# Performance work log

Hardware: AMD Instinct MI355X
Metric: run time of the kernel (lower is better)

The kernel has to match this reference:

```python
import jax, jax.numpy as jnp
import numpy as np

N_NODES = 50000


def _gin_conv(x, src, dst, w1, b1, w2, b2):
    # sum-aggregate neighbor features: agg[i] = sum_{(j->i) in E} x[j]
    agg = jax.ops.segment_sum(x[src], dst, num_segments=N_NODES)
    h = x + agg  # eps = 0 (PyG GINConv default, not trainable)
    h = jnp.maximum(h @ w1 + b1, 0.0) @ w2 + b2
    return h


def setup_inputs() -> dict:
    key = jax.random.key(0)
    ks = jax.random.split(key, 10)
    d_in, d_h, d_out = 128, 256, 2
    E = 600000
    x = jax.random.normal(ks[0], (N_NODES, d_in), dtype=jnp.float32)
    edge_index = jax.random.randint(ks[1], (2, E), 0, N_NODES, dtype=jnp.int64)
    s = lambda k, sh: jax.random.normal(k, sh, dtype=jnp.float32) * (1.0 / np.sqrt(sh[0]))
    return {
        "x": x,
        "edge_index": edge_index,
        "w1": s(ks[2], (d_in, d_h)), "b1": jnp.zeros((d_h,), jnp.float32),
        "w2": s(ks[3], (d_h, d_h)), "b2": jnp.zeros((d_h,), jnp.float32),
        "w3": s(ks[4], (d_h, d_h)), "b3": jnp.zeros((d_h,), jnp.float32),
        "w4": s(ks[5], (d_h, d_out)), "b4": jnp.zeros((d_out,), jnp.float32),
    }


def reference(x, edge_index, w1, b1, w2, b2, w3, b3, w4, b4):
    src, dst = edge_index[0], edge_index[1]
    h = _gin_conv(x, src, dst, w1, b1, w2, b2)
    h = jnp.maximum(h, 0.0)  # F.relu between the two GINConv layers
    h = _gin_conv(h, src, dst, w3, b3, w4, b4)
    return jax.nn.log_softmax(h, axis=1)
```

## Files before the change

kernel.cpp:

```cpp
#include <hip/hip_runtime.h>
#include <hip/hip_bf16.h>


typedef __attribute__((ext_vector_type(8))) short bf16x8;
typedef __attribute__((ext_vector_type(4))) float f32x4;

static __device__ __forceinline__ unsigned short f2bf(float f) {
    unsigned int u = __float_as_uint(f);
    unsigned int r = (u + 0x7fffu + ((u >> 16) & 1u)) >> 16;
    return (unsigned short)r;
}
static __device__ __forceinline__ float bf2f(unsigned short s) {
    return __uint_as_float(((unsigned int)s) << 16);
}
static __device__ __forceinline__ float bflo(unsigned int u) {
    return __uint_as_float(u << 16);
}
static __device__ __forceinline__ float bfhi(unsigned int u) {
    return __uint_as_float(u & 0xffff0000u);
}

#define S1 136
#define S2 264

static __device__ __forceinline__ void acc8(float* a, uint2 v, float ss) {
    a[0] = fmaf(ss, (float)( v.x        & 0xff), a[0]);
    a[1] = fmaf(ss, (float)((v.x >> 8 ) & 0xff), a[1]);
    a[2] = fmaf(ss, (float)((v.x >> 16) & 0xff), a[2]);
    a[3] = fmaf(ss, (float)( v.x >> 24        ), a[3]);
    a[4] = fmaf(ss, (float)( v.y        & 0xff), a[4]);
    a[5] = fmaf(ss, (float)((v.y >> 8 ) & 0xff), a[5]);
    a[6] = fmaf(ss, (float)((v.y >> 16) & 0xff), a[6]);
    a[7] = fmaf(ss, (float)( v.y >> 24        ), a[7]);
}

__global__ __launch_bounds__(256) void prep_kernel(
    const float* __restrict__ x,
    unsigned char* __restrict__ x_q, float* __restrict__ xscale,
    const float* __restrict__ w1, const float* __restrict__ w2, const float* __restrict__ w3,
    short* __restrict__ w1t, short* __restrict__ w2t, short* __restrict__ w3t,
    const int* __restrict__ dst, int* __restrict__ deg,
    int M, int E, int cB)
{
    const int b = blockIdx.x;
    const int t = threadIdx.x;
    if (b < cB) {
        const int i = b * 256 + t;
        const int n4 = M * 32;
        if (i >= n4) return;
        const float4 v = *(const float4*)(x + (size_t)i * 4);
        float mx = fmaxf(fmaxf(fabsf(v.x), fabsf(v.y)), fmaxf(fabsf(v.z), fabsf(v.w)));
        #pragma unroll
        for (int o2 = 1; o2 < 32; o2 <<= 1)
            mx = fmaxf(mx, __shfl_xor(mx, o2));
        const float inv = (mx > 0.f) ? 127.f / mx : 0.f;
        uchar4 o;
        o.x = (unsigned char)(int)(v.x * inv + 128.5f);
        o.y = (unsigned char)(int)(v.y * inv + 128.5f);
        o.z = (unsigned char)(int)(v.z * inv + 128.5f);
        o.w = (unsigned char)(int)(v.w * inv + 128.5f);
        const int row = i >> 5;
        *(uchar4*)(x_q + (size_t)row * 128 + (i & 31) * 4) = o;
        if ((t & 31) == 0) xscale[row] = (mx > 0.f) ? mx * (1.f / 127.f) : 0.f;
        return;
    }
    if (b < cB + 192) {
        const int tb = b - cB;
        const int z = tb >> 6;
        const int rem = tb & 63;
        const int kb = rem & 7;
        const int nb = rem >> 3;
        const float* in; short* outb; int K, ostride;
        if (z == 0)      { in = w1; outb = w1t; K = 128; ostride = S1; }
        else if (z == 1) { in = w2; outb = w2t; K = 256; ostride = S2; }
        else             { in = w3; outb = w3t; K = 256; ostride = S2; }
        const int N = 256;
        const int k0 = kb * 32;
        if (k0 >= K) return;
        const int n0 = nb * 32;
        __shared__ float tile[32][33];
        const int tx = t & 31;
        const int ty = t >> 5;
        #pragma unroll
        for (int i = 0; i < 4; ++i)
            tile[ty + 8 * i][tx] = in[(size_t)(k0 + ty + 8 * i) * N + n0 + tx];
        __syncthreads();
        #pragma unroll
        for (int i = 0; i < 4; ++i)
            outb[(size_t)(n0 + ty + 8 * i) * ostride + k0 + tx] = (short)f2bf(tile[tx][ty + 8 * i]);
        return;
    }
    const int e = (b - cB - 192) * 256 + t;
    if (e < E) atomicAdd(&deg[dst[e]], 1);
}

__global__ __launch_bounds__(256) void block_sum_kernel(
    const int* __restrict__ deg, int* __restrict__ bsum, int M)
{
    const int b = blockIdx.x, t = threadIdx.x;
    const int idx = b * 1024 + t * 4;
    int s = 0;
    if (idx + 3 < M) {
        const int4 v = *(const int4*)(deg + idx);
        s = v.x + v.y + v.z + v.w;
    } else {
        #pragma unroll
        for (int i = 0; i < 4; ++i) if (idx + i < M) s += deg[idx + i];
    }
    #pragma unroll
    for (int off = 32; off > 0; off >>= 1) s += __shfl_down(s, off);
    __shared__ int ws[4];
    if ((t & 63) == 0) ws[t >> 6] = s;
    __syncthreads();
    if (t == 0) bsum[b] = ws[0] + ws[1] + ws[2] + ws[3];
}

__global__ __launch_bounds__(256) void scan_blocks2_kernel(
    const int* __restrict__ deg, const int* __restrict__ bsum,
    int* __restrict__ rowptr, int* __restrict__ cur, int M, int E, int nB)
{
    const int b = blockIdx.x, t = threadIdx.x;
    __shared__ int sboff;
    if (t < 64) {
        const int v = (t < nB) ? bsum[t] : 0;
        int inc = v;
        #pragma unroll
        for (int off = 1; off < 64; off <<= 1) {
            const int u = __shfl_up(inc, off);
            if (t >= off) inc += u;
        }
        const int prev = __shfl(inc, (b == 0) ? 0 : (b - 1));
        if (t == 0) sboff = (b == 0) ? 0 : prev;
    }
    const int idx = b * 1024 + t * 4;
    int4 d = make_int4(0, 0, 0, 0);
    if (idx + 3 < M) {
        d = *(const int4*)(deg + idx);
    } else {
        if (idx + 0 < M) d.x = deg[idx + 0];
        if (idx + 1 < M) d.y = deg[idx + 1];
        if (idx + 2 < M) d.z = deg[idx + 2];
        if (idx + 3 < M) d.w = deg[idx + 3];
    }
    const int tot = d.x + d.y + d.z + d.w;
    const int lane = t & 63, wid = t >> 6;
    int inc = tot;
    #pragma unroll
    for (int off = 1; off < 64; off <<= 1) {
        const int u = __shfl_up(inc, off);
        if (lane >= off) inc += u;
    }
    __shared__ int wsum[4];
    if (lane == 63) wsum[wid] = inc;
    __syncthreads();
    int woff = 0;
    #pragma unroll
    for (int w = 0; w < 4; ++w) if (w < wid) woff += wsum[w];
    int p = sboff + woff + (inc - tot);
    if (idx + 0 < M) { rowptr[idx + 0] = p; cur[idx + 0] = p; } p += d.x;
    if (idx + 1 < M) { rowptr[idx + 1] = p; cur[idx + 1] = p; } p += d.y;
    if (idx + 2 < M) { rowptr[idx + 2] = p; cur[idx + 2] = p; } p += d.z;
    if (idx + 3 < M) { rowptr[idx + 3] = p; cur[idx + 3] = p; }
    if (b == 0 && t == 0) rowptr[M] = E;
}

__global__ __launch_bounds__(256) void fill_kernel(
    const int* __restrict__ src, const int* __restrict__ dst,
    int* __restrict__ cur, int* __restrict__ srcs, int E)
{
    const int e = blockIdx.x * 256 + threadIdx.x;
    if (e >= E) return;
    const int p = atomicAdd(&cur[dst[e]], 1);
    srcs[p] = src[e];
}

__global__ __launch_bounds__(256) void gather_add_d128q(
    const unsigned char* __restrict__ x_q,
    const float* __restrict__ xscale,
    const int* __restrict__ rowptr, const int* __restrict__ srcs,
    short* __restrict__ outb, int M)
{
    const int row = blockIdx.x * 4 + (threadIdx.x >> 6);
    if (row >= M) return;
    const int lane = threadIdx.x & 63;
    const int qt = lane >> 4;
    const int o = (lane & 15) * 8;
    float a[8];
    #pragma unroll
    for (int k = 0; k < 8; ++k) a[k] = 0.f;
    float ssum = 0.f;
    if (qt == 0) {
        const uint2 u = *(const uint2*)(x_q + (size_t)row * 128 + o);
        const float sc = xscale[row];
        acc8(a, u, sc);
        ssum += sc;
    }
    const int jb = rowptr[row], je = rowptr[row + 1];
    for (int j = jb; j < je; j += 16) {
        int ss[4];
        #pragma unroll
        for (int t = 0; t < 4; ++t)
            ss[t] = srcs[min(j + 4 * t + qt, je - 1)];
        uint2 v[4]; float sc[4];
        #pragma unroll
        for (int t = 0; t < 4; ++t) {
            v[t] = *(const uint2*)(x_q + (size_t)ss[t] * 128 + o);
            const float scv = xscale[ss[t]];
            sc[t] = (j + 4 * t + qt < je) ? scv : 0.f;
        }
        #pragma unroll
        for (int t = 0; t < 4; ++t) { acc8(a, v[t], sc[t]); ssum += sc[t]; }
    }
    #pragma unroll
    for (int k = 0; k < 8; ++k) a[k] = fmaf(-128.f, ssum, a[k]);
    #pragma unroll
    for (int k = 0; k < 8; ++k) {
        a[k] += __shfl_down(a[k], 16);
        a[k] += __shfl_down(a[k], 32);
    }
    if (qt == 0) {
        uint4 up;
        up.x = (unsigned int)f2bf(a[0]) | ((unsigned int)f2bf(a[1]) << 16);
        up.y = (unsigned int)f2bf(a[2]) | ((unsigned int)f2bf(a[3]) << 16);
        up.z = (unsigned int)f2bf(a[4]) | ((unsigned int)f2bf(a[5]) << 16);
        up.w = (unsigned int)f2bf(a[6]) | ((unsigned int)f2bf(a[7]) << 16);
        *(uint4*)(outb + (size_t)row * S1 + o) = up;
    }
}

__global__ __launch_bounds__(256) void gather_add_d256q(
    const unsigned char* __restrict__ h1q,
    const float* __restrict__ hscale,
    const int* __restrict__ rowptr, const int* __restrict__ srcs,
    short* __restrict__ outb, int M)
{
    const int row = blockIdx.x * 4 + (threadIdx.x >> 6);
    if (row >= M) return;
    const int lane = threadIdx.x & 63;
    const int half = lane >> 5;
    const int o = (lane & 31) * 8;
    float a[8];
    #pragma unroll
    for (int k = 0; k < 8; ++k) a[k] = 0.f;
    if (half == 0) {
        const uint2 u = *(const uint2*)(h1q + (size_t)row * 256 + o);
        acc8(a, u, hscale[row]);
    }
    const int jb = rowptr[row], je = rowptr[row + 1];
    for (int j = jb; j < je; j += 16) {
        int ss[8];
        #pragma unroll
        for (int t = 0; t < 8; ++t)
            ss[t] = srcs[min(j + 2 * t + half, je - 1)];
        uint2 v[8]; float sc[8];
        #pragma unroll
        for (int t = 0; t < 8; ++t) {
            v[t] = *(const uint2*)(h1q + (size_t)ss[t] * 256 + o);
            const float scv = hscale[ss[t]];
            sc[t] = (j + 2 * t + half < je) ? scv : 0.f;
        }
        #pragma unroll
        for (int t = 0; t < 8; ++t) acc8(a, v[t], sc[t]);
    }
    #pragma unroll
    for (int k = 0; k < 8; ++k) a[k] += __shfl_down(a[k], 32);
    if (half == 0) {
        uint4 up;
        up.x = (unsigned int)f2bf(a[0]) | ((unsigned int)f2bf(a[1]) << 16);
        up.y = (unsigned int)f2bf(a[2]) | ((unsigned int)f2bf(a[3]) << 16);
        up.z = (unsigned int)f2bf(a[4]) | ((unsigned int)f2bf(a[5]) << 16);
        up.w = (unsigned int)f2bf(a[6]) | ((unsigned int)f2bf(a[7]) << 16);
        *(uint4*)(outb + (size_t)row * S2 + o) = up;
    }
}

__global__ __launch_bounds__(256) void layer1_fused(
    const short* __restrict__ h1in,
    const short* __restrict__ w1t,
    const float* __restrict__ b1,
    const short* __restrict__ w2t,
    const float* __restrict__ b2,
    unsigned char* __restrict__ h1q,
    float* __restrict__ hscale,
    int M)
{
    __shared__ short sT[64 * S2];
    __shared__ float sMax[64][4];
    __shared__ float sInv[64];
    const int tid  = threadIdx.x;
    const int lane = tid & 63;
    const int wid  = tid >> 6;
    const int r16  = lane & 15;
    const int q    = lane >> 4;
    const int tm   = blockIdx.x * 64;
    const int wn   = wid * 64;

    {
        const short* Aslice = h1in + (size_t)tm * S1;
        #pragma unroll
        for (int c = 0; c < 5; ++c) {
            const int idx = tid + c * 256;
            if (idx < 64 * S1 / 8) {
                const uint4 v = *(const uint4*)(Aslice + idx * 8);
                *(uint4*)(&sT[idx * 8]) = v;
            }
        }
    }
    __syncthreads();

    f32x4 acc[4][4];
    #pragma unroll
    for (int i = 0; i < 4; ++i)
        #pragma unroll
        for (int j = 0; j < 4; ++j)
            acc[i][j] = (f32x4)0.f;

    #pragma unroll
    for (int k0 = 0; k0 < 128; k0 += 32) {
        bf16x8 af[4], bfr[4];
        #pragma unroll
        for (int i = 0; i < 4; ++i)
            af[i] = *(const bf16x8*)(&sT[(i * 16 + r16) * S1 + k0 + q * 8]);
        #pragma unroll
        for (int j = 0; j < 4; ++j)
            bfr[j] = *(const bf16x8*)(w1t + (size_t)(wn + j * 16 + r16) * S1 + k0 + q * 8);
        #pragma unroll
        for (int i = 0; i < 4; ++i)
            #pragma unroll
            for (int j = 0; j < 4; ++j)
                acc[i][j] = __builtin_amdgcn_mfma_f32_16x16x32_bf16(af[i], bfr[j], acc[i][j], 0, 0, 0);
    }
    __syncthreads();

    #pragma unroll
    for (int j = 0; j < 4; ++j) {
        const int col = wn + j * 16 + r16;
        const float bj = b1[col];
        #pragma unroll
        for (int i = 0; i < 4; ++i)
            #pragma unroll
            for (int r = 0; r < 4; ++r) {
                float v = fmaxf(acc[i][j][r] + bj, 0.f);
                sT[(i * 16 + q * 4 + r) * S2 + col] = (short)f2bf(v);
            }
    }
    __syncthreads();

    #pragma unroll
    for (int i = 0; i < 4; ++i)
        #pragma unroll
        for (int j = 0; j < 4; ++j)
            acc[i][j] = (f32x4)0.f;

    #pragma unroll
    for (int k0 = 0; k0 < 256; k0 += 32) {
        bf16x8 af[4], bfr[4];
        #pragma unroll
        for (int i = 0; i < 4; ++i)
            af[i] = *(const bf16x8*)(&sT[(i * 16 + r16) * S2 + k0 + q * 8]);
        #pragma unroll
        for (int j = 0; j < 4; ++j)
            bfr[j] = *(const bf16x8*)(w2t + (size_t)(wn + j * 16 + r16) * S2 + k0 + q * 8);
        #pragma unroll
        for (int i = 0; i < 4; ++i)
            #pragma unroll
            for (int j = 0; j < 4; ++j)
                acc[i][j] = __builtin_amdgcn_mfma_f32_16x16x32_bf16(af[i], bfr[j], acc[i][j], 0, 0, 0);
    }
    __syncthreads();

    {
        float bj4[4];
        #pragma unroll
        for (int j = 0; j < 4; ++j) bj4[j] = b2[wn + j * 16 + r16];
        #pragma unroll
        for (int i = 0; i < 4; ++i) {
            #pragma unroll
            for (int r = 0; r < 4; ++r) {
                float m = 0.f;
                #pragma unroll
                for (int j = 0; j < 4; ++j) {
                    float v = fmaxf(acc[i][j][r] + bj4[j], 0.f);
                    sT[(i * 16 + q * 4 + r) * S2 + wn + j * 16 + r16] = (short)f2bf(v);
                    m = fmaxf(m, v);
                }
                #pragma unroll
                for (int off = 1; off < 16; off <<= 1)
                    m = fmaxf(m, __shfl_xor(m, off));
                if (r16 == 0) sMax[i * 16 + q * 4 + r][wid] = m;
            }
        }
    }
    __syncthreads();

    if (tid < 64) {
        const float m = fmaxf(fmaxf(sMax[tid][0], sMax[tid][1]),
                              fmaxf(sMax[tid][2], sMax[tid][3]));
        sInv[tid] = (m > 0.f) ? 255.f / m : 0.f;
        const int rg = tm + tid;
        if (rg < M) hscale[rg] = m * (1.f / 255.f);
    }
    __syncthreads();

    #pragma unroll
    for (int c = 0; c < 8; ++c) {
        const int idx = tid + c * 256;
        const int row = idx >> 5;
        const int ch  = idx & 31;
        const int rg  = tm + row;
        if (rg < M) {
            const uint4 v = *(const uint4*)(&sT[row * S2 + ch * 8]);
            const float inv = sInv[row];
            unsigned int q0 = min(255u, (unsigned int)(bflo(v.x) * inv + 0.5f));
            unsigned int q1 = min(255u, (unsigned int)(bfhi(v.x) * inv + 0.5f));
            unsigned int q2 = min(255u, (unsigned int)(bflo(v.y) * inv + 0.5f));
            unsigned int q3 = min(255u, (unsigned int)(bfhi(v.y) * inv + 0.5f));
            unsigned int q4 = min(255u, (unsigned int)(bflo(v.z) * inv + 0.5f));
            unsigned int q5 = min(255u, (unsigned int)(bfhi(v.z) * inv + 0.5f));
            unsigned int q6 = min(255u, (unsigned int)(bflo(v.w) * inv + 0.5f));
            unsigned int q7 = min(255u, (unsigned int)(bfhi(v.w) * inv + 0.5f));
            uint2 o8;
            o8.x = q0 | (q1 << 8) | (q2 << 16) | (q3 << 24);
            o8.y = q4 | (q5 << 8) | (q6 << 16) | (q7 << 24);
            *(uint2*)(h1q + (size_t)rg * 256 + ch * 8) = o8;
        }
    }
}

__global__ __launch_bounds__(256) void layer2_fused(
    const short* __restrict__ h2in,
    const short* __restrict__ w3t,
    const float* __restrict__ b3,
    const float* __restrict__ w4,
    const float* __restrict__ b4,
    float* __restrict__ out,
    int M)
{
    __shared__ short sT[64 * S2];
    const int tid  = threadIdx.x;
    const int lane = tid & 63;
    const int wid  = tid >> 6;
    const int r16  = lane & 15;
    const int q    = lane >> 4;
    const int tm   = blockIdx.x * 64;
    const int wn   = wid * 64;

    {
        const short* Aslice = h2in + (size_t)tm * S2;
        #pragma unroll
        for (int c = 0; c < 9; ++c) {
            const int idx = tid + c * 256;
            if (idx < 64 * S2 / 8) {
                const uint4 v = *(const uint4*)(Aslice + idx * 8);
                *(uint4*)(&sT[idx * 8]) = v;
            }
        }
    }
    __syncthreads();

    f32x4 acc[4][4];
    #pragma unroll
    for (int i = 0; i < 4; ++i)
        #pragma unroll
        for (int j = 0; j < 4; ++j)
            acc[i][j] = (f32x4)0.f;

    #pragma unroll
    for (int k0 = 0; k0 < 256; k0 += 32) {
        bf16x8 af[4], bfr[4];
        #pragma unroll
        for (int i = 0; i < 4; ++i)
            af[i] = *(const bf16x8*)(&sT[(i * 16 + r16) * S2 + k0 + q * 8]);
        #pragma unroll
        for (int j = 0; j < 4; ++j)
            bfr[j] = *(const bf16x8*)(w3t + (size_t)(wn + j * 16 + r16) * S2 + k0 + q * 8);
        #pragma unroll
        for (int i = 0; i < 4; ++i)
            #pragma unroll
            for (int j = 0; j < 4; ++j)
                acc[i][j] = __builtin_amdgcn_mfma_f32_16x16x32_bf16(af[i], bfr[j], acc[i][j], 0, 0, 0);
    }
    __syncthreads();

    #pragma unroll
    for (int j = 0; j < 4; ++j) {
        const int col = wn + j * 16 + r16;
        const float bj = b3[col];
        #pragma unroll
        for (int i = 0; i < 4; ++i)
            #pragma unroll
            for (int r = 0; r < 4; ++r) {
                float v = fmaxf(acc[i][j][r] + bj, 0.f);
                sT[(i * 16 + q * 4 + r) * S2 + col] = (short)f2bf(v);
            }
    }
    __syncthreads();

    const int row = tid >> 2;
    const int qd  = tid & 3;
    const short* tp = &sT[row * S2 + qd * 64];
    const float* w4p = w4 + qd * 128;
    float s0 = 0.f, s1 = 0.f;
    #pragma unroll 8
    for (int k = 0; k < 64; ++k) {
        const float a = bf2f((unsigned short)tp[k]);
        const float2 w = *(const float2*)(w4p + 2 * k);
        s0 = fmaf(a, w.x, s0);
        s1 = fmaf(a, w.y, s1);
    }
    s0 += __shfl_down(s0, 2, 4);  s1 += __shfl_down(s1, 2, 4);
    s0 += __shfl_down(s0, 1, 4);  s1 += __shfl_down(s1, 1, 4);
    if (qd == 0) {
        const int rg = tm + row;
        if (rg < M) {
            s0 += b4[0];
            s1 += b4[1];
            const float m = fmaxf(s0, s1);
            const float l = logf(__expf(s0 - m) + __expf(s1 - m));
            float2 o;
            o.x = s0 - m - l;
            o.y = s1 - m - l;
            *(float2*)(out + (size_t)rg * 2) = o;
        }
    }
}

extern "C" void kernel_launch(void* const* d_in, const int* in_sizes, int n_in,
                              void* d_out, int out_size, void* d_ws, size_t ws_size,
                              hipStream_t stream)
{
    const float* x  = (const float*)d_in[0];
    const int*   ei = (const int*)d_in[1];
    const float* w1 = (const float*)d_in[2];
    const float* b1 = (const float*)d_in[3];
    const float* w2 = (const float*)d_in[4];
    const float* b2 = (const float*)d_in[5];
    const float* w3 = (const float*)d_in[6];
    const float* b3 = (const float*)d_in[7];
    const float* w4 = (const float*)d_in[8];
    const float* b4 = (const float*)d_in[9];

    const int DIN = 128, DH = 256;
    const int M = in_sizes[0] / DIN;
    const int E = in_sizes[1] / 2;
    const int* src = ei;
    const int* dst = ei + E;
    const int nB = (M + 1023) / 1024;

    int* deg    = (int*)d_ws;
    int* bsum   = deg + M;
    int* cur    = bsum + 64;
    int* rowptr = cur + M;
    int* srcs   = rowptr + (M + 1);
    size_t off = ((size_t)(3 * M + 1 + 64 + E) * sizeof(int) + 255) & ~(size_t)255;
    unsigned char* x_q = (unsigned char*)((char*)d_ws + off);  off += (size_t)M * 128;
    off = (off + 255) & ~(size_t)255;
    float* xscale = (float*)((char*)d_ws + off);  off += (size_t)M * 4;
    off = (off + 255) & ~(size_t)255;
    short* h1in = (short*)((char*)d_ws + off);  off += (size_t)M * S1 * 2;
    off = (off + 255) & ~(size_t)255;
    unsigned char* h1q = (unsigned char*)((char*)d_ws + off);  off += (size_t)M * 256;
    off = (off + 255) & ~(size_t)255;
    float* hscale = (float*)((char*)d_ws + off);  off += (size_t)M * 4;
    off = (off + 255) & ~(size_t)255;
    short* h2in = (short*)((char*)d_ws + off);  off += (size_t)M * S2 * 2;
    off = (off + 255) & ~(size_t)255;
    short* w1t  = (short*)((char*)d_ws + off);  off += (size_t)DH * S1 * 2;
    off = (off + 255) & ~(size_t)255;
    short* w2t  = (short*)((char*)d_ws + off);  off += (size_t)DH * S2 * 2;
    off = (off + 255) & ~(size_t)255;
    short* w3t  = (short*)((char*)d_ws + off);  off += (size_t)DH * S2 * 2;

    hipMemsetAsync(deg, 0, (size_t)M * sizeof(int), stream);
    const int cB = (M * 32 + 255) / 256;
    const int dB = (E + 255) / 256;
    prep_kernel<<<cB + 192 + dB, 256, 0, stream>>>(
        x, x_q, xscale, w1, w2, w3, w1t, w2t, w3t, dst, deg, M, E, cB);

    block_sum_kernel<<<nB, 256, 0, stream>>>(deg, bsum, M);
    scan_blocks2_kernel<<<nB, 256, 0, stream>>>(deg, bsum, rowptr, cur, M, E, nB);
    fill_kernel<<<dB, 256, 0, stream>>>(src, dst, cur, srcs, E);

    const int nblk = (M + 63) / 64;

    gather_add_d128q<<<(M + 3) / 4, 256, 0, stream>>>(x_q, xscale, rowptr, srcs, h1in, M);
    layer1_fused<<<nblk, 256, 0, stream>>>(h1in, w1t, b1, w2t, b2, h1q, hscale, M);

    gather_add_d256q<<<(M + 3) / 4, 256, 0, stream>>>(h1q, hscale, rowptr, srcs, h2in, M);
    layer2_fused<<<nblk, 256, 0, stream>>>(h2in, w3t, b3, w4, b4, (float*)d_out, M);
}
```

Measured before the change: 271.8 us.

## Fuse neighbor gather-aggregation into layer MLP kernels via shared memory

Moves the sparse gather-sum for each layer into the corresponding fused MLP kernel, so each block aggregates its 64 rows directly into shared memory instead of writing bf16 intermediates to global memory and reading them back. This removes two kernel launches and the global round-trip of the h1in/h2in buffers. In exchange, each wave now processes 16 rows serially with less parallelism per row and fewer concurrent memory requests in flight, and the gather's latency is no longer overlapped by a separate high-occupancy kernel.

```diff
diff --git a/kernel.cpp b/kernel.cpp
--- a/kernel.cpp
+++ b/kernel.cpp
@@ -174,108 +174,10 @@
     srcs[p] = src[e];
 }
 
-__global__ __launch_bounds__(256) void gather_add_d128q(
+__global__ __launch_bounds__(256) void layer1_fused(
     const unsigned char* __restrict__ x_q,
     const float* __restrict__ xscale,
     const int* __restrict__ rowptr, const int* __restrict__ srcs,
-    short* __restrict__ outb, int M)
-{
-    const int row = blockIdx.x * 4 + (threadIdx.x >> 6);
-    if (row >= M) return;
-    const int lane = threadIdx.x & 63;
-    const int qt = lane >> 4;
-    const int o = (lane & 15) * 8;
-    float a[8];
-    #pragma unroll
-    for (int k = 0; k < 8; ++k) a[k] = 0.f;
-    float ssum = 0.f;
-    if (qt == 0) {
-        const uint2 u = *(const uint2*)(x_q + (size_t)row * 128 + o);
-        const float sc = xscale[row];
-        acc8(a, u, sc);
-        ssum += sc;
-    }
-    const int jb = rowptr[row], je = rowptr[row + 1];
-    for (int j = jb; j < je; j += 16) {
-        int ss[4];
-        #pragma unroll
-        for (int t = 0; t < 4; ++t)
-            ss[t] = srcs[min(j + 4 * t + qt, je - 1)];
-        uint2 v[4]; float sc[4];
-        #pragma unroll
-        for (int t = 0; t < 4; ++t) {
-            v[t] = *(const uint2*)(x_q + (size_t)ss[t] * 128 + o);
-            const float scv = xscale[ss[t]];
-            sc[t] = (j + 4 * t + qt < je) ? scv : 0.f;
-        }
-        #pragma unroll
-        for (int t = 0; t < 4; ++t) { acc8(a, v[t], sc[t]); ssum += sc[t]; }
-    }
-    #pragma unroll
-    for (int k = 0; k < 8; ++k) a[k] = fmaf(-128.f, ssum, a[k]);
-    #pragma unroll
-    for (int k = 0; k < 8; ++k) {
-        a[k] += __shfl_down(a[k], 16);
-        a[k] += __shfl_down(a[k], 32);
-    }
-    if (qt == 0) {
-        uint4 up;
-        up.x = (unsigned int)f2bf(a[0]) | ((unsigned int)f2bf(a[1]) << 16);
-        up.y = (unsigned int)f2bf(a[2]) | ((unsigned int)f2bf(a[3]) << 16);
-        up.z = (unsigned int)f2bf(a[4]) | ((unsigned int)f2bf(a[5]) << 16);
-        up.w = (unsigned int)f2bf(a[6]) | ((unsigned int)f2bf(a[7]) << 16);
-        *(uint4*)(outb + (size_t)row * S1 + o) = up;
-    }
-}
-
-__global__ __launch_bounds__(256) void gather_add_d256q(
-    const unsigned char* __restrict__ h1q,
-    const float* __restrict__ hscale,
-    const int* __restrict__ rowptr, const int* __restrict__ srcs,
-    short* __restrict__ outb, int M)
-{
-    const int row = blockIdx.x * 4 + (threadIdx.x >> 6);
-    if (row >= M) return;
-    const int lane = threadIdx.x & 63;
-    const int half = lane >> 5;
-    const int o = (lane & 31) * 8;
-    float a[8];
-    #pragma unroll
-    for (int k = 0; k < 8; ++k) a[k] = 0.f;
-    if (half == 0) {
-        const uint2 u = *(const uint2*)(h1q + (size_t)row * 256 + o);
-        acc8(a, u, hscale[row]);
-    }
-    const int jb = rowptr[row], je = rowptr[row + 1];
-    for (int j = jb; j < je; j += 16) {
-        int ss[8];
-        #pragma unroll
-        for (int t = 0; t < 8; ++t)
-            ss[t] = srcs[min(j + 2 * t + half, je - 1)];
-        uint2 v[8]; float sc[8];
-        #pragma unroll
-        for (int t = 0; t < 8; ++t) {
-            v[t] = *(const uint2*)(h1q + (size_t)ss[t] * 256 + o);
-            const float scv = hscale[ss[t]];
-            sc[t] = (j + 2 * t + half < je) ? scv : 0.f;
-        }
-        #pragma unroll
-        for (int t = 0; t < 8; ++t) acc8(a, v[t], sc[t]);
-    }
-    #pragma unroll
-    for (int k = 0; k < 8; ++k) a[k] += __shfl_down(a[k], 32);
-    if (half == 0) {
-        uint4 up;
-        up.x = (unsigned int)f2bf(a[0]) | ((unsigned int)f2bf(a[1]) << 16);
-        up.y = (unsigned int)f2bf(a[2]) | ((unsigned int)f2bf(a[3]) << 16);
-        up.z = (unsigned int)f2bf(a[4]) | ((unsigned int)f2bf(a[5]) << 16);
-        up.w = (unsigned int)f2bf(a[6]) | ((unsigned int)f2bf(a[7]) << 16);
-        *(uint4*)(outb + (size_t)row * S2 + o) = up;
-    }
-}
-
-__global__ __launch_bounds__(256) void layer1_fused(
-    const short* __restrict__ h1in,
     const short* __restrict__ w1t,
     const float* __restrict__ b1,
     const short* __restrict__ w2t,
@@ -296,13 +198,53 @@
     const int wn   = wid * 64;
 
     {
-        const short* Aslice = h1in + (size_t)tm * S1;
-        #pragma unroll
-        for (int c = 0; c < 5; ++c) {
-            const int idx = tid + c * 256;
-            if (idx < 64 * S1 / 8) {
-                const uint4 v = *(const uint4*)(Aslice + idx * 8);
-                *(uint4*)(&sT[idx * 8]) = v;
+        const int qt = lane >> 4;
+        const int o  = (lane & 15) * 8;
+        for (int r = 0; r < 16; ++r) {
+            const int lr   = wid * 16 + r;
+            const int grow = tm + lr;
+            float a[8];
+            #pragma unroll
+            for (int k = 0; k < 8; ++k) a[k] = 0.f;
+            float ssum = 0.f;
+            if (grow < M) {
+                if (qt == 0) {
+                    const uint2 u = *(const uint2*)(x_q + (size_t)grow * 128 + o);
+                    const float sc = xscale[grow];
+                    acc8(a, u, sc);
+                    ssum += sc;
+                }
+                const int jb = rowptr[grow], je = rowptr[grow + 1];
+                for (int j = jb; j < je; j += 16) {
+                    int ss[4];
+                    #pragma unroll
+                    for (int t = 0; t < 4; ++t)
+                        ss[t] = srcs[min(j + 4 * t + qt, je - 1)];
+                    uint2 v[4]; float sc[4];
+                    #pragma unroll
+                    for (int t = 0; t < 4; ++t) {
+                        v[t] = *(const uint2*)(x_q + (size_t)ss[t] * 128 + o);
+                        const float scv = xscale[ss[t]];
+                        sc[t] = (j + 4 * t + qt < je) ? scv : 0.f;
+                    }
+                    #pragma unroll
+                    for (int t = 0; t < 4; ++t) { acc8(a, v[t], sc[t]); ssum += sc[t]; }
+                }
+                #pragma unroll
+                for (int k = 0; k < 8; ++k) a[k] = fmaf(-128.f, ssum, a[k]);
+            }
+            #pragma unroll
+            for (int k = 0; k < 8; ++k) {
+                a[k] += __shfl_down(a[k], 16);
+                a[k] += __shfl_down(a[k], 32);
+            }
+            if (qt == 0) {
+                uint4 up;
+                up.x = (unsigned int)f2bf(a[0]) | ((unsigned int)f2bf(a[1]) << 16);
+                up.y = (unsigned int)f2bf(a[2]) | ((unsigned int)f2bf(a[3]) << 16);
+                up.z = (unsigned int)f2bf(a[4]) | ((unsigned int)f2bf(a[5]) << 16);
+                up.w = (unsigned int)f2bf(a[6]) | ((unsigned int)f2bf(a[7]) << 16);
+                *(uint4*)(&sT[lr * S1 + o]) = up;
             }
         }
     }
@@ -428,7 +370,9 @@
 }
 
 __global__ __launch_bounds__(256) void layer2_fused(
-    const short* __restrict__ h2in,
+    const unsigned char* __restrict__ h1q,
+    const float* __restrict__ hscale,
+    const int* __restrict__ rowptr, const int* __restrict__ srcs,
     const short* __restrict__ w3t,
     const float* __restrict__ b3,
     const float* __restrict__ w4,
@@ -446,13 +390,45 @@
     const int wn   = wid * 64;
 
     {
-        const short* Aslice = h2in + (size_t)tm * S2;
-        #pragma unroll
-        for (int c = 0; c < 9; ++c) {
-            const int idx = tid + c * 256;
-            if (idx < 64 * S2 / 8) {
-                const uint4 v = *(const uint4*)(Aslice + idx * 8);
-                *(uint4*)(&sT[idx * 8]) = v;
+        const int half = lane >> 5;
+        const int o    = (lane & 31) * 8;
+        for (int r = 0; r < 16; ++r) {
+            const int lr   = wid * 16 + r;
+            const int grow = tm + lr;
+            float a[8];
+            #pragma unroll
+            for (int k = 0; k < 8; ++k) a[k] = 0.f;
+            if (grow < M) {
+                if (half == 0) {
+                    const uint2 u = *(const uint2*)(h1q + (size_t)grow * 256 + o);
+                    acc8(a, u, hscale[grow]);
+                }
+                const int jb = rowptr[grow], je = rowptr[grow + 1];
+                for (int j = jb; j < je; j += 16) {
+                    int ss[8];
+                    #pragma unroll
+                    for (int t = 0; t < 8; ++t)
+                        ss[t] = srcs[min(j + 2 * t + half, je - 1)];
+                    uint2 v[8]; float sc[8];
+                    #pragma unroll
+                    for (int t = 0; t < 8; ++t) {
+                        v[t] = *(const uint2*)(h1q + (size_t)ss[t] * 256 + o);
+                        const float scv = hscale[ss[t]];
+                        sc[t] = (j + 2 * t + half < je) ? scv : 0.f;
+                    }
+                    #pragma unroll
+                    for (int t = 0; t < 8; ++t) acc8(a, v[t], sc[t]);
+                }
+            }
+            #pragma unroll
+            for (int k = 0; k < 8; ++k) a[k] += __shfl_down(a[k], 32);
+            if (half == 0) {
+                uint4 up;
+                up.x = (unsigned int)f2bf(a[0]) | ((unsigned int)f2bf(a[1]) << 16);
+                up.y = (unsigned int)f2bf(a[2]) | ((unsigned int)f2bf(a[3]) << 16);
+                up.z = (unsigned int)f2bf(a[4]) | ((unsigned int)f2bf(a[5]) << 16);
+                up.w = (unsigned int)f2bf(a[6]) | ((unsigned int)f2bf(a[7]) << 16);
+                *(uint4*)(&sT[lr * S2 + o]) = up;
             }
         }
     }
@@ -557,13 +533,9 @@
     off = (off + 255) & ~(size_t)255;
     float* xscale = (float*)((char*)d_ws + off);  off += (size_t)M * 4;
     off = (off + 255) & ~(size_t)255;
-    short* h1in = (short*)((char*)d_ws + off);  off += (size_t)M * S1 * 2;
-    off = (off + 255) & ~(size_t)255;
     unsigned char* h1q = (unsigned char*)((char*)d_ws + off);  off += (size_t)M * 256;
     off = (off + 255) & ~(size_t)255;
     float* hscale = (float*)((char*)d_ws + off);  off += (size_t)M * 4;
-    off = (off + 255) & ~(size_t)255;
-    short* h2in = (short*)((char*)d_ws + off);  off += (size_t)M * S2 * 2;
     off = (off + 255) & ~(size_t)255;
     short* w1t  = (short*)((char*)d_ws + off);  off += (size_t)DH * S1 * 2;
     off = (off + 255) & ~(size_t)255;
@@ -583,9 +555,9 @@
 
     const int nblk = (M + 63) / 64;
 
-    gather_add_d128q<<<(M + 3) / 4, 256, 0, stream>>>(x_q, xscale, rowptr, srcs, h1in, M);
-    layer1_fused<<<nblk, 256, 0, stream>>>(h1in, w1t, b1, w2t, b2, h1q, hscale, M);
-
-    gather_add_d256q<<<(M + 3) / 4, 256, 0, stream>>>(h1q, hscale, rowptr, srcs, h2in, M);
-    layer2_fused<<<nblk, 256, 0, stream>>>(h2in, w3t, b3, w4, b4, (float*)d_out, M);
-}
+    layer1_fused<<<nblk, 256, 0, stream>>>(
+        x_q, xscale, rowptr, srcs, w1t, b1, w2t, b2, h1q, hscale, M);
+
+    layer2_fused<<<nblk, 256, 0, stream>>>(
+        h1q, hscale, rowptr, srcs, w3t, b3, w4, b4, (float*)d_out, M);
+}
```

After: 315.0 us. +15.9%, slower.
